# Kernel optimization log

Hardware: AMD Instinct MI355X
Metric: run time of the kernel (lower is better)

The kernel has to match this reference:

```python
import jax, jax.numpy as jnp
import numpy as np

ALPHA = 0.2  # LeakyReLU negative slope
NEG_INF = -1e12


def setup_inputs() -> dict:
    key = jax.random.key(0)
    k1, k2, k3, k4, k5 = jax.random.split(key, 5)
    N, F = 4096, 512
    inp = jax.random.normal(k1, (N, F), dtype=jnp.float32)
    adj = jax.random.randint(k2, (N, N), 0, 2).astype(jnp.float32)
    W = jax.random.normal(k3, (F, F), dtype=jnp.float32) * (1.414 / np.sqrt(F))
    a = jax.random.normal(k4, (2 * F, 1), dtype=jnp.float32) * 0.05
    wtrans = jax.random.normal(k5, (2 * F, F), dtype=jnp.float32) * (1.414 / np.sqrt(1.5 * F))
    return {"inp": inp, "adj": adj, "W": W, "a": a, "wtrans": wtrans}


def reference(inp, adj, W, a, wtrans):
    F_out = W.shape[1]
    h = inp @ W                                   # [N, F]
    Wh1 = h @ a[:F_out, :]                        # [N, 1]
    Wh2 = h @ a[F_out:, :]                        # [N, 1]
    e = jax.nn.leaky_relu(Wh1 + Wh2.T, ALPHA)     # [N, N]
    mask = adj > 0
    attention = jax.nn.softmax(jnp.where(mask, e, NEG_INF), axis=1)
    negative_attention = -jax.nn.softmax(jnp.where(mask, -e, NEG_INF), axis=1)
    # dropout p=0.0 (eval mode): identity
    h_prime = attention @ inp                     # [N, F_in]
    h_prime_negative = negative_attention @ inp   # [N, F_in]
    h_prime_double = jnp.concatenate([h_prime, h_prime_negative], axis=1)
    new_h_prime = h_prime_double @ wtrans         # [N, F_out]
    return jax.nn.elu(new_h_prime)
```

## Files before the change

kernel.cpp:

```cpp
#include <hip/hip_runtime.h>
#include <hip/hip_bf16.h>

#define N_NODES 4096
#define F_DIM   512
#define KTOT    8192
#define KSPLIT  8
#define LOG2E   1.44269504f

typedef __attribute__((ext_vector_type(8))) short bf16x8;
typedef __attribute__((ext_vector_type(4))) float f32x4;

__device__ inline unsigned short f2bf(float f) {
  union { float f; unsigned u; } c; c.f = f;
  unsigned r = c.u + 0x7fffu + ((c.u >> 16) & 1u);
  return (unsigned short)(r >> 16);
}
__device__ inline float bf2f(unsigned short u) {
  union { unsigned u; float f; } c; c.u = ((unsigned)u) << 16;
  return c.f;
}

__global__ void k_compute_v(const float* __restrict__ W, const float* __restrict__ a,
                            float* __restrict__ v1, float* __restrict__ v2) {
  int r = blockIdx.x, l = threadIdx.x;
  float s1 = 0.f, s2 = 0.f;
  for (int c = l; c < F_DIM; c += 64) {
    float w = W[(size_t)r * F_DIM + c];
    s1 += w * a[c];
    s2 += w * a[F_DIM + c];
  }
#pragma unroll
  for (int off = 32; off > 0; off >>= 1) { s1 += __shfl_down(s1, off); s2 += __shfl_down(s2, off); }
  if (l == 0) { v1[r] = s1; v2[r] = s2; }
}

__global__ void k_compute_wh(const float* __restrict__ inp, const float* __restrict__ v1,
                             const float* __restrict__ v2, float* __restrict__ Wh1,
                             float* __restrict__ Wh2) {
  int i = blockIdx.x, l = threadIdx.x;
  float s1 = 0.f, s2 = 0.f;
  for (int c = l; c < F_DIM; c += 64) {
    float x = inp[(size_t)i * F_DIM + c];
    s1 += x * v1[c];
    s2 += x * v2[c];
  }
#pragma unroll
  for (int off = 32; off > 0; off >>= 1) { s1 += __shfl_down(s1, off); s2 += __shfl_down(s2, off); }
  if (l == 0) { Wh1[i] = s1 * LOG2E; Wh2[i] = s2 * LOG2E; }
}

__global__ void k_transpose_bf16(const float* __restrict__ src, unsigned short* __restrict__ dst,
                                 int R, int C) {
  __shared__ float tile[32][33];
  int c0 = blockIdx.x * 32, r0 = blockIdx.y * 32;
  int tx = threadIdx.x, ty = threadIdx.y;
#pragma unroll
  for (int i = ty; i < 32; i += 8)
    tile[i][tx] = src[(size_t)(r0 + i) * C + c0 + tx];
  __syncthreads();
#pragma unroll
  for (int i = ty; i < 32; i += 8)
    dst[(size_t)(c0 + i) * R + r0 + tx] = f2bf(tile[tx][i]);
}

__global__ __launch_bounds__(256) void k_y(const float* __restrict__ inp,
                                           const unsigned short* __restrict__ wtT,
                                           unsigned short* __restrict__ YT) {
  int tid = threadIdx.x, l = tid & 63, w = tid >> 6;
  int row = l & 15, kg = l >> 4;
  int jt = blockIdx.x * 64 + w * 16;
  int cb = blockIdx.y * 64;
  f32x4 acc1[4] = {}, acc2[4] = {};
  const float* ap = inp + (size_t)(jt + row) * F_DIM + kg * 8;
  for (int k0 = 0; k0 < F_DIM; k0 += 32) {
    float4 f0 = *(const float4*)(ap + k0);
    float4 f1 = *(const float4*)(ap + k0 + 4);
    bf16x8 a;
    a[0] = (short)f2bf(f0.x); a[1] = (short)f2bf(f0.y); a[2] = (short)f2bf(f0.z); a[3] = (short)f2bf(f0.w);
    a[4] = (short)f2bf(f1.x); a[5] = (short)f2bf(f1.y); a[6] = (short)f2bf(f1.z); a[7] = (short)f2bf(f1.w);
#pragma unroll
    for (int n = 0; n < 4; n++) {
      const unsigned short* bp = wtT + (size_t)(cb + n * 16 + row) * 1024 + kg * 8 + k0;
      bf16x8 b1 = *(const bf16x8*)(bp);
      bf16x8 b2 = *(const bf16x8*)(bp + F_DIM);
      acc1[n] = __builtin_amdgcn_mfma_f32_16x16x32_bf16(a, b1, acc1[n], 0, 0, 0);
      acc2[n] = __builtin_amdgcn_mfma_f32_16x16x32_bf16(a, b2, acc2[n], 0, 0, 0);
    }
  }
  int jb = jt + kg * 4;
#pragma unroll
  for (int n = 0; n < 4; n++) {
    int f = cb + n * 16 + row;
    ushort4 o1, o2;
    o1.x = f2bf(acc1[n][0]); o1.y = f2bf(acc1[n][1]); o1.z = f2bf(acc1[n][2]); o1.w = f2bf(acc1[n][3]);
    o2.x = f2bf(acc2[n][0]); o2.y = f2bf(acc2[n][1]); o2.z = f2bf(acc2[n][2]); o2.w = f2bf(acc2[n][3]);
    *(ushort4*)(YT + (size_t)f * KTOT + jb) = o1;
    *(ushort4*)(YT + (size_t)f * KTOT + 4096 + jb) = o2;
  }
}

__global__ __launch_bounds__(256) void k_p(const float* __restrict__ adj,
                                           const float* __restrict__ Wh1,
                                           const float* __restrict__ Wh2,
                                           unsigned short* __restrict__ Pcat) {
  int i = blockIdx.x, t = threadIdx.x;
  float w1 = Wh1[i];
  int j0 = t * 16;
  const float* ar = adj + (size_t)i * N_NODES + j0;
  float4 A0 = *(const float4*)(ar);
  float4 A1 = *(const float4*)(ar + 4);
  float4 A2 = *(const float4*)(ar + 8);
  float4 A3 = *(const float4*)(ar + 12);
  float am[16] = {A0.x, A0.y, A0.z, A0.w, A1.x, A1.y, A1.z, A1.w,
                  A2.x, A2.y, A2.z, A2.w, A3.x, A3.y, A3.z, A3.w};
  float4 wv0 = *(const float4*)(Wh2 + j0);
  float4 wv1 = *(const float4*)(Wh2 + j0 + 4);
  float4 wv2 = *(const float4*)(Wh2 + j0 + 8);
  float4 wv3 = *(const float4*)(Wh2 + j0 + 12);
  float w2[16] = {wv0.x, wv0.y, wv0.z, wv0.w, wv1.x, wv1.y, wv1.z, wv1.w,
                  wv2.x, wv2.y, wv2.z, wv2.w, wv3.x, wv3.y, wv3.z, wv3.w};
  float pe[16], ne[16];
  float sp = 0.f, sn = 0.f;
#pragma unroll
  for (int r = 0; r < 16; r++) {
    float s = w1 + w2[r];
    float e = fmaxf(s, 0.2f * s);
    float p = exp2f(e);
    float n = exp2f(-e);
    if (!(am[r] > 0.f)) { p = 0.f; n = 0.f; }
    pe[r] = p; ne[r] = n; sp += p; sn += n;
  }
#pragma unroll
  for (int off = 1; off < 64; off <<= 1) { sp += __shfl_xor(sp, off); sn += __shfl_xor(sn, off); }
  __shared__ float red[2][4];
  int wv = t >> 6, ln = t & 63;
  if (ln == 0) { red[0][wv] = sp; red[1][wv] = sn; }
  __syncthreads();
  sp = red[0][0] + red[0][1] + red[0][2] + red[0][3];
  sn = red[1][0] + red[1][1] + red[1][2] + red[1][3];
  float rp = 1.f / sp;
  float rn = -1.f / sn;
  bf16x8 o;
#pragma unroll
  for (int r = 0; r < 8; r++) o[r] = (short)f2bf(pe[r] * rp);
  *(bf16x8*)(Pcat + (size_t)i * KTOT + j0) = o;
#pragma unroll
  for (int r = 0; r < 8; r++) o[r] = (short)f2bf(pe[8 + r] * rp);
  *(bf16x8*)(Pcat + (size_t)i * KTOT + j0 + 8) = o;
#pragma unroll
  for (int r = 0; r < 8; r++) o[r] = (short)f2bf(ne[r] * rn);
  *(bf16x8*)(Pcat + (size_t)i * KTOT + 4096 + j0) = o;
#pragma unroll
  for (int r = 0; r < 8; r++) o[r] = (short)f2bf(ne[8 + r] * rn);
  *(bf16x8*)(Pcat + (size_t)i * KTOT + 4096 + j0 + 8) = o;
}

#define GLOAD16(gp, lp) __builtin_amdgcn_global_load_lds( \
    (const __attribute__((address_space(1))) unsigned int*)(gp), \
    (__attribute__((address_space(3))) unsigned int*)(lp), 16, 0, 0)

__global__ __launch_bounds__(512, 1) void k_pv(const unsigned short* __restrict__ Pcat,
                                               const unsigned short* __restrict__ YT,
                                               unsigned short* __restrict__ part) {
  __shared__ char ldsA[65536];
  __shared__ char ldsB[65536];
  int t = threadIdx.x;
  int l = t & 63, w = t >> 6;
  int la = l & 15, kg = l >> 4;
  int wr = w >> 2, wc = w & 3;
  int bm0 = blockIdx.x * 256, bn0 = blockIdx.y * 256;
  int z = blockIdx.z;
  size_t zoffB = (size_t)z * (KTOT / KSPLIT) * 2;

  int lgq = ((t & 7) ^ ((t >> 3) & 7)) << 4;
  const char* gPc = (const char*)Pcat + (size_t)(bm0 + (t >> 3)) * (KTOT * 2) + zoffB + lgq;
  const char* gYt = (const char*)YT  + (size_t)(bn0 + (t >> 3)) * (KTOT * 2) + zoffB + lgq;

#define STA(T, q) GLOAD16(gPc + (size_t)(q) * 64 * (KTOT * 2) + (size_t)(T) * 128, \
                          ldsA + ((T) & 1) * 32768 + ((q) >> 1) * 16384 + ((q) & 1) * 8192 + w * 1024)
#define STB(T, u) GLOAD16(gYt + (size_t)(u) * 64 * (KTOT * 2) + (size_t)(T) * 128, \
                          ldsB + ((T) & 1) * 32768 + ((u) >> 1) * 16384 + ((u) & 1) * 8192 + w * 1024)

  f32x4 acc[8][4] = {};
  bf16x8 af[4], bfr[2][4];

#define PHASE(D, RH, KS, READB, STAGES, VMC) do { \
  const char* Ah_ = ldsA + (D) * 32768 + wr * 16384 + (RH) * 64 * 128; \
  _Pragma("unroll") for (int mi = 0; mi < 4; mi++) \
    af[mi] = *(const bf16x8*)(Ah_ + (mi * 16 + la) * 128 + ((((KS) * 4 + kg)) ^ (la & 7)) * 16); \
  if (READB) { \
    const char* Bh_ = ldsB + (D) * 32768 + (wc >> 1) * 16384; \
    _Pragma("unroll") for (int ni = 0; ni < 4; ni++) \
      bfr[KS][ni] = *(const bf16x8*)(Bh_ + ((wc & 1) * 64 + ni * 16 + la) * 128 + ((((KS) * 4 + kg)) ^ (la & 7)) * 16); \
  } \
  STAGES; \
  VMC; \
  __builtin_amdgcn_s_barrier(); \
  asm volatile("s_waitcnt lgkmcnt(0)" ::: "memory"); \
  __builtin_amdgcn_sched_barrier(0); \
  __builtin_amdgcn_s_setprio(1); \
  _Pragma("unroll") for (int mi = 0; mi < 4; mi++) \
    _Pragma("unroll") for (int ni = 0; ni < 4; ni++) \
      acc[(RH) * 4 + mi][ni] = __builtin_amdgcn_mfma_f32_16x16x32_bf16(af[mi], bfr[KS][ni], acc[(RH) * 4 + mi][ni], 0, 0, 0); \
  __builtin_amdgcn_s_setprio(0); \
  __builtin_amdgcn_s_barrier(); \
} while (0)

  STA(0, 0); STA(0, 1); STA(0, 2); STA(0, 3);
  STB(0, 0); STB(0, 1); STB(0, 2); STB(0, 3);
  STA(1, 0); STA(1, 1); STA(1, 2); STA(1, 3);
  STB(1, 0); STB(1, 1); STB(1, 2); STB(1, 3);
  asm volatile("s_waitcnt vmcnt(8)" ::: "memory");
  __builtin_amdgcn_s_barrier();

  for (int it = 0; it < 8; ++it) {
    int T1 = 2 * it + 1, T2 = 2 * it + 2, T3 = 2 * it + 3;
    bool mid = (it > 0), more = (it < 7);
    PHASE(0, 0, 0, true,  { if (mid) { STA(T1, 1); STA(T1, 3); } }, {});
    PHASE(0, 0, 1, true,  { if (mid) { STB(T1, 0); STB(T1, 1); } }, {});
    PHASE(0, 1, 0, false, { if (mid) { STB(T1, 2); STB(T1, 3); } }, {});
    PHASE(0, 1, 1, false, { if (more) { STA(T2, 0); STA(T2, 2); } },
          { if (more) asm volatile("s_waitcnt vmcnt(2)" ::: "memory");
            else      asm volatile("s_waitcnt vmcnt(0)" ::: "memory"); });
    PHASE(1, 0, 0, true,  { if (more) { STA(T2, 1); STA(T2, 3); } }, {});
    PHASE(1, 0, 1, true,  { if (more) { STB(T2, 0); STB(T2, 1); } }, {});
    PHASE(1, 1, 0, false, { if (more) { STB(T2, 2); STB(T2, 3); } }, {});
    PHASE(1, 1, 1, false, { if (more) { STA(T3, 0); STA(T3, 2); } },
          { if (more) asm volatile("s_waitcnt vmcnt(2)" ::: "memory");
            else      asm volatile("s_waitcnt vmcnt(0)" ::: "memory"); });
  }

  unsigned short* po = part + (size_t)z * (N_NODES * F_DIM);
#pragma unroll
  for (int rh = 0; rh < 2; rh++)
#pragma unroll
    for (int mi = 0; mi < 4; mi++)
#pragma unroll
      for (int ni = 0; ni < 4; ni++)
#pragma unroll
        for (int q = 0; q < 4; q++) {
          int i_ = bm0 + wr * 128 + rh * 64 + mi * 16 + kg * 4 + q;
          int f_ = bn0 + wc * 64 + ni * 16 + la;
          po[(size_t)i_ * F_DIM + f_] = f2bf(acc[rh * 4 + mi][ni][q]);
        }
}

__global__ __launch_bounds__(256) void k_fin(const unsigned short* __restrict__ part,
                                             float* __restrict__ out) {
  size_t idx = ((size_t)blockIdx.x * 256 + threadIdx.x) * 8;
  float s[8] = {};
#pragma unroll
  for (int p = 0; p < KSPLIT; p++) {
    bf16x8 v = *(const bf16x8*)(part + (size_t)p * (N_NODES * F_DIM) + idx);
#pragma unroll
    for (int q = 0; q < 8; q++) s[q] += bf2f((unsigned short)v[q]);
  }
#pragma unroll
  for (int q = 0; q < 8; q++) s[q] = s[q] > 0.f ? s[q] : (__expf(s[q]) - 1.f);
  float4 o0 = make_float4(s[0], s[1], s[2], s[3]);
  float4 o1 = make_float4(s[4], s[5], s[6], s[7]);
  *(float4*)(out + idx) = o0;
  *(float4*)(out + idx + 4) = o1;
}

extern "C" void kernel_launch(void* const* d_in, const int* in_sizes, int n_in,
                              void* d_out, int out_size, void* d_ws, size_t ws_size,
                              hipStream_t stream) {
  (void)in_sizes; (void)n_in; (void)out_size; (void)ws_size;
  const float* inp    = (const float*)d_in[0];
  const float* adj    = (const float*)d_in[1];
  const float* W      = (const float*)d_in[2];
  const float* a      = (const float*)d_in[3];
  const float* wtrans = (const float*)d_in[4];
  float* out = (float*)d_out;

  char* ws = (char*)d_ws;
  float* v1  = (float*)ws;
  float* v2  = (float*)(ws + 2048);
  float* Wh1 = (float*)(ws + 4096);
  float* Wh2 = (float*)(ws + 20480);

  const size_t PSZ = (size_t)N_NODES * F_DIM * 2;
  char* regA = ws + 65536;
  unsigned short* wtT  = (unsigned short*)regA;
  unsigned short* part = (unsigned short*)regA;
  unsigned short* YT   = (unsigned short*)(regA + KSPLIT * PSZ);
  unsigned short* Pcat = (unsigned short*)(regA + KSPLIT * PSZ + 8388608);

  k_compute_v<<<512, 64, 0, stream>>>(W, a, v1, v2);
  k_compute_wh<<<4096, 64, 0, stream>>>(inp, v1, v2, Wh1, Wh2);
  k_transpose_bf16<<<dim3(16, 32), dim3(32, 8), 0, stream>>>(wtrans, wtT, 1024, F_DIM);
  k_y<<<dim3(64, 8), 256, 0, stream>>>(inp, wtT, YT);
  k_p<<<4096, 256, 0, stream>>>(adj, Wh1, Wh2, Pcat);
  k_pv<<<dim3(16, 2, KSPLIT), 512, 0, stream>>>(Pcat, YT, part);
  k_fin<<<1024, 256, 0, stream>>>(part, out);
}
```

Baseline: 122.5 us.

## Rebalance GEMM prefetch schedule and stage partial-sum epilogue through LDS

```diff
diff --git a/kernel.cpp b/kernel.cpp
--- a/kernel.cpp
+++ b/kernel.cpp
@@ -184,7 +184,7 @@
   f32x4 acc[8][4] = {};
   bf16x8 af[4], bfr[2][4];
 
-#define PHASE(D, RH, KS, READB, STAGES, VMC) do { \
+#define PHASE(D, RH, KS, READB, WAITC, STAGES) do { \
   const char* Ah_ = ldsA + (D) * 32768 + wr * 16384 + (RH) * 64 * 128; \
   _Pragma("unroll") for (int mi = 0; mi < 4; mi++) \
     af[mi] = *(const bf16x8*)(Ah_ + (mi * 16 + la) * 128 + ((((KS) * 4 + kg)) ^ (la & 7)) * 16); \
@@ -193,8 +193,8 @@
     _Pragma("unroll") for (int ni = 0; ni < 4; ni++) \
       bfr[KS][ni] = *(const bf16x8*)(Bh_ + ((wc & 1) * 64 + ni * 16 + la) * 128 + ((((KS) * 4 + kg)) ^ (la & 7)) * 16); \
   } \
+  WAITC; \
   STAGES; \
-  VMC; \
   __builtin_amdgcn_s_barrier(); \
   asm volatile("s_waitcnt lgkmcnt(0)" ::: "memory"); \
   __builtin_amdgcn_sched_barrier(0); \
@@ -215,34 +215,54 @@
 
   for (int it = 0; it < 8; ++it) {
     int T1 = 2 * it + 1, T2 = 2 * it + 2, T3 = 2 * it + 3;
-    bool mid = (it > 0), more = (it < 7);
-    PHASE(0, 0, 0, true,  { if (mid) { STA(T1, 1); STA(T1, 3); } }, {});
-    PHASE(0, 0, 1, true,  { if (mid) { STB(T1, 0); STB(T1, 1); } }, {});
-    PHASE(0, 1, 0, false, { if (mid) { STB(T1, 2); STB(T1, 3); } }, {});
-    PHASE(0, 1, 1, false, { if (more) { STA(T2, 0); STA(T2, 2); } },
-          { if (more) asm volatile("s_waitcnt vmcnt(2)" ::: "memory");
-            else      asm volatile("s_waitcnt vmcnt(0)" ::: "memory"); });
-    PHASE(1, 0, 0, true,  { if (more) { STA(T2, 1); STA(T2, 3); } }, {});
-    PHASE(1, 0, 1, true,  { if (more) { STB(T2, 0); STB(T2, 1); } }, {});
-    PHASE(1, 1, 0, false, { if (more) { STB(T2, 2); STB(T2, 3); } }, {});
-    PHASE(1, 1, 1, false, { if (more) { STA(T3, 0); STA(T3, 2); } },
-          { if (more) asm volatile("s_waitcnt vmcnt(2)" ::: "memory");
-            else      asm volatile("s_waitcnt vmcnt(0)" ::: "memory"); });
-  }
-
-  unsigned short* po = part + (size_t)z * (N_NODES * F_DIM);
-#pragma unroll
-  for (int rh = 0; rh < 2; rh++)
-#pragma unroll
-    for (int mi = 0; mi < 4; mi++)
-#pragma unroll
-      for (int ni = 0; ni < 4; ni++)
-#pragma unroll
-        for (int q = 0; q < 4; q++) {
-          int i_ = bm0 + wr * 128 + rh * 64 + mi * 16 + kg * 4 + q;
-          int f_ = bn0 + wc * 64 + ni * 16 + la;
-          po[(size_t)i_ * F_DIM + f_] = f2bf(acc[rh * 4 + mi][ni][q]);
-        }
+    bool pre = (it > 0), more = (it < 7);
+    PHASE(0, 0, 0, true,  {}, { if (pre)  { STA(T1, 1); STA(T1, 3); } });
+    PHASE(0, 0, 1, true,  {}, {});
+    PHASE(0, 1, 0, false, {}, { if (more) { STA(T2, 0); STA(T2, 2); STB(T2, 0); STB(T2, 1); } });
+    PHASE(0, 1, 1, false,
+          { if (more) asm volatile("s_waitcnt vmcnt(4)" ::: "memory");
+            else      asm volatile("s_waitcnt vmcnt(0)" ::: "memory"); },
+          { if (more) { STB(T2, 2); STB(T2, 3); } });
+    PHASE(1, 0, 0, true,  {}, { if (more) { STA(T2, 1); STA(T2, 3); } });
+    PHASE(1, 0, 1, true,  {}, {});
+    PHASE(1, 1, 0, false, {}, { if (more) { STA(T3, 0); STA(T3, 2); STB(T3, 0); STB(T3, 1); STB(T3, 2); STB(T3, 3); } });
+    PHASE(1, 1, 1, false,
+          { if (more) asm volatile("s_waitcnt vmcnt(6)" ::: "memory");
+            else      asm volatile("s_waitcnt vmcnt(0)" ::: "memory"); },
+          {});
+  }
+
+  {
+#pragma unroll
+    for (int rh = 0; rh < 2; rh++)
+#pragma unroll
+      for (int mi = 0; mi < 4; mi++)
+#pragma unroll
+        for (int ni = 0; ni < 4; ni++)
+#pragma unroll
+          for (int q = 0; q < 4; q++) {
+            int r = wr * 128 + rh * 64 + mi * 16 + kg * 4 + q;
+            int cb2 = (wc * 64 + ni * 16 + la) * 2;
+            char* base = (r < 128) ? (ldsA + r * 512) : (ldsB + (r - 128) * 512);
+            *(unsigned short*)(base + (cb2 ^ (((r >> 2) & 3) << 4))) =
+                f2bf(acc[rh * 4 + mi][ni][q]);
+          }
+    __builtin_amdgcn_s_barrier();
+    unsigned short* po = part + (size_t)z * (N_NODES * F_DIM);
+#pragma unroll
+    for (int pass = 0; pass < 4; pass++) {
+      int r2 = pass * 64 + w * 8 + (l >> 3);
+      const char* rb = (r2 < 128) ? (ldsA + r2 * 512) : (ldsB + (r2 - 128) * 512);
+      int xm = ((r2 >> 2) & 3) << 4;
+      char* gout = (char*)(po + (size_t)(bm0 + r2) * F_DIM + bn0) + (l & 7) * 64;
+#pragma unroll
+      for (int g = 0; g < 4; g++) {
+        int off = (l & 7) * 64 + g * 16;
+        f32x4 v = *(const f32x4*)(rb + (off ^ xm));
+        *(f32x4*)(gout + g * 16) = v;
+      }
+    }
+  }
 }
 
 __global__ __launch_bounds__(256) void k_fin(const unsigned short* __restrict__ part,
```

Measured after the change: 130.1 us. 1.06x slower.
